# Performance work log

Measured on AMD Instinct MI355X. Metric: run time of the kernel, lower is better.

## Reference

```python
import jax, jax.numpy as jnp
import numpy as np

NUM_EXPERTS = 8
TOP_K = 2

def setup_inputs() -> dict:
    key = jax.random.key(0)
    ks = jax.random.split(key, 5)
    B, S, D, E, H = 4, 2048, 1024, NUM_EXPERTS, 4096
    scale = 0.02
    return {
        'x': jax.random.normal(ks[0], (B, S, D), dtype=jnp.float32),
        'router_w': jax.random.normal(ks[1], (D, E), dtype=jnp.float32) * scale,
        'router_b': jnp.zeros((E,), dtype=jnp.float32),
        'w1': jax.random.normal(ks[2], (E, D, H), dtype=jnp.float32) * scale,
        'b1': jnp.zeros((E, H), dtype=jnp.float32),
        'w2': jax.random.normal(ks[3], (E, H, D), dtype=jnp.float32) * scale,
        'b2': jnp.zeros((E, D), dtype=jnp.float32),
    }

def reference(x, router_w, router_b, w1, b1, w2, b2):
    B, S, D = x.shape
    E = router_b.shape[0]
    x_flat = x.reshape(-1, D)                       # [T, D], T = B*S
    logits = x_flat @ router_w + router_b          # [T, E]
    routing_weights = jax.nn.softmax(logits, axis=-1)
    # NOTE: original module computes & renormalizes top-k weights but never
    # applies them — outputs of selected experts are summed UNWEIGHTED.
    top_w, top_idx = jax.lax.top_k(routing_weights, TOP_K)  # [T, k]
    out_flat = jnp.zeros_like(x_flat)
    for e in range(E):  # fixed small expert count; dense compute + mask combine
        mask = jnp.any(top_idx == e, axis=-1)      # [T]
        h = jax.nn.gelu(x_flat @ w1[e] + b1[e], approximate=False)  # [T, H]
        y = h @ w2[e] + b2[e]                      # [T, D]
        out_flat = out_flat + jnp.where(mask[:, None], y, 0.0)
    return out_flat.reshape(B, S, D)
```

## Files before the change

### kernel.cpp

```cpp
#include <hip/hip_runtime.h>

#define T_TOKENS 8192
#define DIM 1024
#define NEXP 8
#define HID 4096
#define ROWS (2 * T_TOKENS)
#define ROWS_PAD (ROWS + 256)

#define META_COUNTS 0
#define META_OFFSET 16
#define META_TOP2   32
#define META_ROWPOS (32 + T_TOKENS)

typedef __attribute__((ext_vector_type(8))) short short8;
typedef __attribute__((ext_vector_type(4))) float f32x4;
typedef __attribute__((ext_vector_type(4))) unsigned short u16x4;

__device__ __forceinline__ unsigned short bf16bits(float f) {
  unsigned u = __builtin_bit_cast(unsigned, f);
  u += 0x7fffu + ((u >> 16) & 1u);
  return (unsigned short)(u >> 16);
}

__device__ __forceinline__ void gl_lds16(const void* g, void* l) {
  __builtin_amdgcn_global_load_lds(
      (const __attribute__((address_space(1))) unsigned int*)g,
      (__attribute__((address_space(3))) unsigned int*)l, 16, 0, 0);
}

__device__ __forceinline__ float gelu_tanh(float x) {
  float x3 = x * x * x;
  float z = 0.7978845608028654f * x + 0.035677408136300125f * x3;
  float az = fabsf(z);
  float e = exp2f(az * 2.885390081777927f);
  float t = 1.0f - 2.0f / (1.0f + e);
  t = copysignf(t, z);
  return 0.5f * x * (1.0f + t);
}

__global__ __launch_bounds__(256) void transpose_w_kernel(
    const float* __restrict__ in, unsigned short* __restrict__ out, int R, int C) {
  __shared__ float tile[64][65];
  const int e = blockIdx.z;
  const int r0 = blockIdx.y * 64, c0 = blockIdx.x * 64;
  const float* inp = in + (size_t)e * R * C;
  unsigned short* outp = out + (size_t)e * R * C;
  const int tr = threadIdx.x >> 4;
  const int tc = (threadIdx.x & 15) * 4;
#pragma unroll
  for (int s = 0; s < 64; s += 16) {
    f32x4 v = *(const f32x4*)(inp + (size_t)(r0 + tr + s) * C + c0 + tc);
    tile[tr + s][tc + 0] = v[0]; tile[tr + s][tc + 1] = v[1];
    tile[tr + s][tc + 2] = v[2]; tile[tr + s][tc + 3] = v[3];
  }
  __syncthreads();
#pragma unroll
  for (int s = 0; s < 64; s += 16) {
    int orow = c0 + tr + s;
    u16x4 u;
#pragma unroll
    for (int k = 0; k < 4; ++k) u[k] = bf16bits(tile[tc + k][tr + s]);
    *(u16x4*)(outp + (size_t)orow * R + r0 + tc) = u;
  }
}

__global__ __launch_bounds__(256) void router_kernel(
    const float* __restrict__ x, const float* __restrict__ rw,
    const float* __restrict__ rb, int* __restrict__ meta) {
  const int w = threadIdx.x >> 6;
  const int l = threadIdx.x & 63;
  const int t = blockIdx.x * 4 + w;
  const float* xr = x + (size_t)t * DIM + l * 16;
  double acc[8];
#pragma unroll
  for (int e = 0; e < 8; ++e) acc[e] = 0.0;
#pragma unroll
  for (int m = 0; m < 16; m += 4) {
    f32x4 xv = *(const f32x4*)(xr + m);
#pragma unroll
    for (int q = 0; q < 4; ++q) {
      double xs = (double)xv[q];
      const float* rwr = rw + (size_t)(l * 16 + m + q) * NEXP;
      f32x4 r0 = *(const f32x4*)rwr;
      f32x4 r1 = *(const f32x4*)(rwr + 4);
      acc[0] += xs * (double)r0[0]; acc[1] += xs * (double)r0[1];
      acc[2] += xs * (double)r0[2]; acc[3] += xs * (double)r0[3];
      acc[4] += xs * (double)r1[0]; acc[5] += xs * (double)r1[1];
      acc[6] += xs * (double)r1[2]; acc[7] += xs * (double)r1[3];
    }
  }
#pragma unroll
  for (int off = 32; off >= 1; off >>= 1) {
#pragma unroll
    for (int e = 0; e < 8; ++e) acc[e] += __shfl_down(acc[e], off);
  }
  if (l == 0) {
    double lg[8];
#pragma unroll
    for (int e = 0; e < 8; ++e) lg[e] = acc[e] + (double)rb[e];
    int e1 = 0; double b1v = lg[0];
#pragma unroll
    for (int e = 1; e < 8; ++e) if (lg[e] > b1v) { b1v = lg[e]; e1 = e; }
    int e2 = -1; double b2v = -1e300;
#pragma unroll
    for (int e = 0; e < 8; ++e) if (e != e1 && lg[e] > b2v) { b2v = lg[e]; e2 = e; }
    meta[META_TOP2 + t] = e1 | (e2 << 4);
  }
}

__global__ __launch_bounds__(1024) void assign_kernel(int* __restrict__ meta) {
  __shared__ int hist[NEXP][1024];
  __shared__ int own[NEXP][1024];
  const int tid = threadIdx.x;
#pragma unroll
  for (int e = 0; e < NEXP; ++e) { hist[e][tid] = 0; own[e][tid] = 0; }
  __syncthreads();
  int top2[8];
#pragma unroll
  for (int q = 0; q < 8; ++q) {
    int t = tid * 8 + q;
    int p = meta[META_TOP2 + t];
    top2[q] = p;
    hist[p & 15][tid] += 1;
    hist[(p >> 4) & 15][tid] += 1;
  }
#pragma unroll
  for (int e = 0; e < NEXP; ++e) own[e][tid] = hist[e][tid];
  __syncthreads();
  for (int off = 1; off < 1024; off <<= 1) {
    int add[NEXP];
#pragma unroll
    for (int e = 0; e < NEXP; ++e) add[e] = (tid >= off) ? hist[e][tid - off] : 0;
    __syncthreads();
#pragma unroll
    for (int e = 0; e < NEXP; ++e) hist[e][tid] += add[e];
    __syncthreads();
  }
  int offp[NEXP];
  {
    int o = 0;
#pragma unroll
    for (int e = 0; e < NEXP; ++e) { offp[e] = o; o += hist[e][1023]; }
  }
  if (tid == 0) {
#pragma unroll
    for (int e = 0; e < NEXP; ++e) {
      meta[META_COUNTS + e] = hist[e][1023];
      meta[META_OFFSET + e] = offp[e];
    }
  }
#pragma unroll
  for (int e = 0; e < NEXP; ++e) own[e][tid] = offp[e] + hist[e][tid] - own[e][tid];
#pragma unroll
  for (int q = 0; q < 8; ++q) {
    int t = tid * 8 + q;
    int p = top2[q];
    int e1 = p & 15, e2 = (p >> 4) & 15;
    int r1 = own[e1][tid]; own[e1][tid] = r1 + 1;
    int r2 = own[e2][tid]; own[e2][tid] = r2 + 1;
    meta[META_ROWPOS + 2 * t] = r1;
    meta[META_ROWPOS + 2 * t + 1] = r2;
  }
}

__global__ __launch_bounds__(256) void gather_kernel(
    const float* __restrict__ x, unsigned short* __restrict__ gx,
    const int* __restrict__ meta) {
  const int t = blockIdx.x;
  const int r1 = meta[META_ROWPOS + 2 * t];
  const int r2 = meta[META_ROWPOS + 2 * t + 1];
  const int i = threadIdx.x * 4;
  f32x4 v = *(const f32x4*)(x + (size_t)t * DIM + i);
  u16x4 u;
  u[0] = bf16bits(v[0]); u[1] = bf16bits(v[1]);
  u[2] = bf16bits(v[2]); u[3] = bf16bits(v[3]);
  *(u16x4*)(gx + (size_t)r1 * DIM + i) = u;
  *(u16x4*)(gx + (size_t)r2 * DIM + i) = u;
}

template <int ACT, int BN, int WAVES_N>
__global__ __launch_bounds__(512) void moe_gemm2ph(
    const unsigned short* __restrict__ A, const unsigned short* __restrict__ Bt,
    const float* __restrict__ bias, void* __restrict__ C,
    const int* __restrict__ meta, int K, int N) {
  constexpr int WAVES_M = 8 / WAVES_N;
  constexpr int MI = 256 / (16 * WAVES_M);
  constexpr int NJ = BN / (16 * WAVES_N);
  constexpr int BPASS = (BN * 64) / 4096;

  const int e = blockIdx.z;
  const int n_e = meta[META_COUNTS + e];
  const int mt = blockIdx.y;
  if (mt * 256 >= n_e) return;
  const int n0 = blockIdx.x * BN;
  const int row0 = meta[META_OFFSET + e] + mt * 256;
  const int mrem = n_e - mt * 256;

  __shared__ __align__(16) unsigned short As[256 * 64];
  __shared__ __align__(16) unsigned short Bs[BN * 64];

  const int tid = threadIdx.x;
  const int wid = tid >> 6, l = tid & 63;
  const int wm = wid / WAVES_N, wn = wid % WAVES_N;
  const int rA = l & 15, cq = l >> 4;

  f32x4 acc[MI][NJ] = {};

  const unsigned short* Ag = A + (size_t)row0 * K;
  const unsigned short* Bg = Bt + (size_t)e * N * K + (size_t)n0 * K;

  for (int kt = 0; kt < K; kt += 64) {
#pragma unroll
    for (int it = 0; it < 4; ++it) {
      int idx = it * 4096 + tid * 8;
      int row = idx >> 6;
      int cp = (idx >> 3) & 7;
      int col = ((cp ^ (row & 7)) << 3);
      gl_lds16(Ag + (size_t)row * K + kt + col, &As[it * 4096 + (wid << 9)]);
    }
#pragma unroll
    for (int it = 0; it < BPASS; ++it) {
      int idx = it * 4096 + tid * 8;
      int row = idx >> 6;
      int cp = (idx >> 3) & 7;
      int col = ((cp ^ (row & 7)) << 3);
      gl_lds16(Bg + (size_t)row * K + kt + col, &Bs[it * 4096 + (wid << 9)]);
    }
    __syncthreads();
#pragma unroll
    for (int ks = 0; ks < 2; ++ks) {
      short8 av[MI], bv[NJ];
      const int c = ks * 4 + cq;
#pragma unroll
      for (int i = 0; i < MI; ++i) {
        int r = wm * (MI * 16) + i * 16 + rA;
        av[i] = *(const short8*)&As[r * 64 + ((c ^ (r & 7)) << 3)];
      }
#pragma unroll
      for (int j = 0; j < NJ; ++j) {
        int r = wn * (NJ * 16) + j * 16 + rA;
        bv[j] = *(const short8*)&Bs[r * 64 + ((c ^ (r & 7)) << 3)];
      }
#pragma unroll
      for (int i = 0; i < MI; ++i)
#pragma unroll
        for (int j = 0; j < NJ; ++j)
          acc[i][j] = __builtin_amdgcn_mfma_f32_16x16x32_bf16(av[i], bv[j], acc[i][j], 0, 0, 0);
    }
    __syncthreads();
  }

  const int lc = l & 15;
  const int lro = (l >> 4) << 2;
#pragma unroll
  for (int i = 0; i < MI; ++i) {
#pragma unroll
    for (int j = 0; j < NJ; ++j) {
      int gn = n0 + wn * (NJ * 16) + j * 16 + lc;
      float bz = bias[(size_t)e * N + gn];
#pragma unroll
      for (int r = 0; r < 4; ++r) {
        int lr = wm * (MI * 16) + i * 16 + lro + r;
        if (lr < mrem) {
          float v = acc[i][j][r] + bz;
          size_t off = (size_t)(row0 + lr) * N + gn;
          if (ACT == 1) {
            ((unsigned short*)C)[off] = bf16bits(gelu_tanh(v));
          } else {
            ((float*)C)[off] = v;
          }
        }
      }
    }
  }
}

__global__ __launch_bounds__(256) void combine_kernel(
    const float* __restrict__ y, const int* __restrict__ meta, float* __restrict__ out) {
  const int t = blockIdx.x;
  const int r1 = meta[META_ROWPOS + 2 * t];
  const int r2 = meta[META_ROWPOS + 2 * t + 1];
  const int i = threadIdx.x * 4;
  f32x4 a = *(const f32x4*)(y + (size_t)r1 * DIM + i);
  f32x4 b = *(const f32x4*)(y + (size_t)r2 * DIM + i);
  f32x4 o = a + b;
  *(f32x4*)(out + (size_t)t * DIM + i) = o;
}

extern "C" void kernel_launch(void* const* d_in, const int* in_sizes, int n_in,
                              void* d_out, int out_size, void* d_ws, size_t ws_size,
                              hipStream_t stream) {
  const float* x  = (const float*)d_in[0];
  const float* rw = (const float*)d_in[1];
  const float* rb = (const float*)d_in[2];
  const float* w1 = (const float*)d_in[3];
  const float* b1 = (const float*)d_in[4];
  const float* w2 = (const float*)d_in[5];
  const float* b2 = (const float*)d_in[6];
  float* out = (float*)d_out;

  char* p = (char*)d_ws;
  unsigned short* w1t = (unsigned short*)p; p += (size_t)NEXP * DIM * HID * 2;
  unsigned short* w2t = (unsigned short*)p; p += (size_t)NEXP * DIM * HID * 2;
  unsigned short* gx  = (unsigned short*)p; p += (size_t)ROWS_PAD * DIM * 2;
  unsigned short* h   = (unsigned short*)p; p += (size_t)ROWS_PAD * HID * 2;
  float*          y   = (float*)p;          p += (size_t)ROWS_PAD * DIM * 4;
  int*            meta = (int*)p;
  (void)in_sizes; (void)n_in; (void)out_size; (void)ws_size;

  transpose_w_kernel<<<dim3(HID / 64, DIM / 64, NEXP), 256, 0, stream>>>(w1, w1t, DIM, HID);
  transpose_w_kernel<<<dim3(DIM / 64, HID / 64, NEXP), 256, 0, stream>>>(w2, w2t, HID, DIM);

  router_kernel<<<T_TOKENS / 4, 256, 0, stream>>>(x, rw, rb, meta);
  assign_kernel<<<1, 1024, 0, stream>>>(meta);
  gather_kernel<<<T_TOKENS, 256, 0, stream>>>(x, gx, meta);

  moe_gemm2ph<1, 256, 4><<<dim3(HID / 256, 32, NEXP), 512, 0, stream>>>(gx, w1t, b1, h, meta, DIM, HID);
  moe_gemm2ph<0, 128, 2><<<dim3(DIM / 128, 32, NEXP), 512, 0, stream>>>(h, w2t, b2, y, meta, HID, DIM);

  combine_kernel<<<T_TOKENS, 256, 0, stream>>>(y, meta, out);
}
```

Measured before the change: 692.6 us.

## Double-buffer LDS tiles in MoE GEMM to overlap global loads with MFMA

```diff
diff --git a/kernel.cpp b/kernel.cpp
--- a/kernel.cpp
+++ b/kernel.cpp
@@ -195,28 +195,27 @@
   const int n0 = blockIdx.x * BN;
   const int row0 = meta[META_OFFSET + e] + mt * 256;
   const int mrem = n_e - mt * 256;
-
-  __shared__ __align__(16) unsigned short As[256 * 64];
-  __shared__ __align__(16) unsigned short Bs[BN * 64];
+  const int NT = K >> 6;
+
+  __shared__ __align__(16) unsigned short As[2][256 * 64];
+  __shared__ __align__(16) unsigned short Bs[2][BN * 64];
 
   const int tid = threadIdx.x;
   const int wid = tid >> 6, l = tid & 63;
   const int wm = wid / WAVES_N, wn = wid % WAVES_N;
   const int rA = l & 15, cq = l >> 4;
 
-  f32x4 acc[MI][NJ] = {};
-
   const unsigned short* Ag = A + (size_t)row0 * K;
   const unsigned short* Bg = Bt + (size_t)e * N * K + (size_t)n0 * K;
 
-  for (int kt = 0; kt < K; kt += 64) {
+  auto stage = [&](int buf, int kt) {
 #pragma unroll
     for (int it = 0; it < 4; ++it) {
       int idx = it * 4096 + tid * 8;
       int row = idx >> 6;
       int cp = (idx >> 3) & 7;
       int col = ((cp ^ (row & 7)) << 3);
-      gl_lds16(Ag + (size_t)row * K + kt + col, &As[it * 4096 + (wid << 9)]);
+      gl_lds16(Ag + (size_t)row * K + kt + col, &As[buf][it * 4096 + (wid << 9)]);
     }
 #pragma unroll
     for (int it = 0; it < BPASS; ++it) {
@@ -224,30 +223,50 @@
       int row = idx >> 6;
       int cp = (idx >> 3) & 7;
       int col = ((cp ^ (row & 7)) << 3);
-      gl_lds16(Bg + (size_t)row * K + kt + col, &Bs[it * 4096 + (wid << 9)]);
-    }
-    __syncthreads();
+      gl_lds16(Bg + (size_t)row * K + kt + col, &Bs[buf][it * 4096 + (wid << 9)]);
+    }
+  };
+
+  stage(0, 0);
+  asm volatile("s_waitcnt vmcnt(0)" ::: "memory");
+  __builtin_amdgcn_s_barrier();
+
+  f32x4 acc[MI][NJ] = {};
+  int cur = 0;
+
+  for (int t = 0; t < NT; ++t) {
+    if (t + 1 < NT) stage(cur ^ 1, (t + 1) << 6);
+    const unsigned short* Ac = As[cur];
+    const unsigned short* Bc = Bs[cur];
+    short8 av[2][MI], bv[2][NJ];
 #pragma unroll
     for (int ks = 0; ks < 2; ++ks) {
-      short8 av[MI], bv[NJ];
       const int c = ks * 4 + cq;
 #pragma unroll
       for (int i = 0; i < MI; ++i) {
         int r = wm * (MI * 16) + i * 16 + rA;
-        av[i] = *(const short8*)&As[r * 64 + ((c ^ (r & 7)) << 3)];
+        av[ks][i] = *(const short8*)&Ac[r * 64 + ((c ^ (r & 7)) << 3)];
       }
 #pragma unroll
       for (int j = 0; j < NJ; ++j) {
         int r = wn * (NJ * 16) + j * 16 + rA;
-        bv[j] = *(const short8*)&Bs[r * 64 + ((c ^ (r & 7)) << 3)];
+        bv[ks][j] = *(const short8*)&Bc[r * 64 + ((c ^ (r & 7)) << 3)];
       }
+    }
+    asm volatile("s_waitcnt lgkmcnt(0)" ::: "memory");
+    __builtin_amdgcn_sched_barrier(0);
+    __builtin_amdgcn_s_setprio(1);
+#pragma unroll
+    for (int ks = 0; ks < 2; ++ks)
 #pragma unroll
       for (int i = 0; i < MI; ++i)
 #pragma unroll
         for (int j = 0; j < NJ; ++j)
-          acc[i][j] = __builtin_amdgcn_mfma_f32_16x16x32_bf16(av[i], bv[j], acc[i][j], 0, 0, 0);
-    }
-    __syncthreads();
+          acc[i][j] = __builtin_amdgcn_mfma_f32_16x16x32_bf16(av[ks][i], bv[ks][j], acc[i][j], 0, 0, 0);
+    __builtin_amdgcn_s_setprio(0);
+    asm volatile("s_waitcnt vmcnt(0)" ::: "memory");
+    __builtin_amdgcn_s_barrier();
+    cur ^= 1;
   }
 
   const int lc = l & 15;
```

Measured after the change: 777.9 us. 12.3% more time.
